# Optimization experiments

Hardware: AMD Instinct MI355X
Metric: run time of the kernel (lower is better)

Reference implementation:

```python
import jax, jax.numpy as jnp
import numpy as np

IN_F = 512
OUT_F = 512
ALPHA = 0.2  # LeakyReLU negative slope
# dropout p=0.1 is a no-op at inference (training=False), so omitted


def setup_inputs() -> dict:
    key = jax.random.key(0)
    k1, k2, k3 = jax.random.split(key, 3)
    B, N = 16, 1024
    x = jax.random.normal(k1, (B, N, IN_F), dtype=jnp.float32)
    # xavier_uniform with gain=1.414
    limW = 1.414 * np.sqrt(6.0 / (IN_F + OUT_F))
    W = jax.random.uniform(k2, (IN_F, OUT_F), minval=-limW, maxval=limW, dtype=jnp.float32)
    lima = 1.414 * np.sqrt(6.0 / (2 * OUT_F + 1))
    a = jax.random.uniform(k3, (2 * OUT_F, 1), minval=-lima, maxval=lima, dtype=jnp.float32)
    beta = jnp.ones((1,), dtype=jnp.float32)
    return {"x": x, "W": W, "a": a, "beta": beta}


def reference(x, W, a, beta):
    # h: [B, N, F]
    h = jnp.matmul(x, W)
    # Split attention vector: e_ij = leakyrelu(h_i . a1 + h_j . a2)
    a1 = a[:OUT_F, 0]   # [F]
    a2 = a[OUT_F:, 0]   # [F]
    s1 = jnp.einsum('bnf,f->bn', h, a1)  # [B, N]
    s2 = jnp.einsum('bnf,f->bn', h, a2)  # [B, N]
    e = s1[:, :, None] + s2[:, None, :]  # [B, N, N]
    e = jnp.where(e > 0, e, ALPHA * e)   # LeakyReLU
    attention = jax.nn.softmax(e, axis=2)
    h_prime = jnp.einsum('bnm,bmf->bnf', attention, h)
    out = jax.nn.elu(h_prime + beta * h)
    return out
```

## Files before the change

kernel.cpp:

```cpp
#include <hip/hip_runtime.h>

using u16 = unsigned short;
using u32 = unsigned int;

#define ALPHA 0.2f
#define LOG2E 1.4426950408889634f

typedef __bf16 bf16x8 __attribute__((ext_vector_type(8)));
typedef float f32x4 __attribute__((ext_vector_type(4)));
typedef float f32x16 __attribute__((ext_vector_type(16)));

__device__ __forceinline__ u16 f2bf(float f) {
  u32 u = __builtin_bit_cast(u32, f);
  u += 0x7FFFu + ((u >> 16) & 1u);
  return (u16)(u >> 16);
}
__device__ __forceinline__ float bf2f(u16 h) {
  u32 u = ((u32)h) << 16;
  return __builtin_bit_cast(float, u);
}
__device__ __forceinline__ void gload_lds16(const void* g, void* l) {
  __builtin_amdgcn_global_load_lds((__attribute__((address_space(1))) void*)g,
                                   (__attribute__((address_space(3))) void*)l,
                                   16, 0, 0);
}

__global__ __launch_bounds__(256) void k_cast_wT(const float* __restrict__ W, u16* __restrict__ wbt) {
  int idx = blockIdx.x * 256 + threadIdx.x;
  int k = idx >> 9, n = idx & 511;
  wbt[n * 512 + k] = f2bf(W[idx]);
}


__global__ __launch_bounds__(256, 2) void k_gemm1(const float* __restrict__ x, const u16* __restrict__ wbt,
                                                  const float* __restrict__ a,
                                                  u16* __restrict__ hbf, u16* __restrict__ hbt2,
                                                  float* __restrict__ s1p, float* __restrict__ s2p) {
  __shared__ __attribute__((aligned(16))) char lds[73728];
  __shared__ __attribute__((aligned(16))) float a_l[256];

  const int t = threadIdx.x;
  const int lane = t & 63;
  const int w = t >> 6;
  const int l31 = lane & 31, lhi = lane >> 5;
  const int rb = w >> 1, cg = w & 1;
  const int g = blockIdx.x;
  const int cb = (g >> 3) & 3;
  const int tile_m = (g & 7) | ((g >> 5) << 3);
  const int row0 = tile_m * 128;
  const int col0 = cb * 128;

  a_l[t] = (t < 128) ? a[col0 + t] : a[512 + col0 + (t - 128)];

  f32x16 acc[2][2];
#pragma unroll
  for (int i = 0; i < 2; ++i)
#pragma unroll
    for (int j = 0; j < 2; ++j)
#pragma unroll
      for (int r = 0; r < 16; ++r) acc[i][j][r] = 0.f;

#define STAGE_G1(kt, Ab, Bb)                                                              \
  {                                                                                       \
    const int k0_ = (kt) * 32;                                                            \
    _Pragma("unroll")                                                                     \
    for (int i = 0; i < 4; ++i) {                                                         \
      int G = i * 256 + t;                                                                \
      int row = G >> 3, ks = G & 7;                                                       \
      gload_lds16(x + (size_t)(row0 + row) * 512 + k0_ + ((ks ^ (row & 7)) * 4),          \
                  (Ab) + (size_t)(i * 256 + w * 64) * 16);                                \
    }                                                                                     \
    _Pragma("unroll")                                                                     \
    for (int i = 0; i < 2; ++i) {                                                         \
      int G = i * 256 + t;                                                                \
      int col = G >> 2, ks = G & 3;                                                       \
      gload_lds16(wbt + (size_t)(col0 + col) * 512 + k0_ + ((ks ^ ((col >> 1) & 3)) * 8), \
                  (Bb) + (size_t)(i * 256 + w * 64) * 16);                                \
    }                                                                                     \
  }

#define COMPUTE_G1(Ab, Bb)                                                                         \
  {                                                                                                \
    _Pragma("unroll")                                                                              \
    for (int ks = 0; ks < 2; ++ks) {                                                               \
      bf16x8 af[2];                                                                                \
      _Pragma("unroll")                                                                            \
      for (int sub = 0; sub < 2; ++sub) {                                                          \
        const int arow = rb * 64 + sub * 32 + l31;                                                 \
        const int kg = ks * 4 + lhi * 2;                                                           \
        f32x4 fa0 = *reinterpret_cast<const f32x4*>((Ab) + (size_t)(arow * 8 + (kg ^ (arow & 7))) * 16); \
        f32x4 fa1 = *reinterpret_cast<const f32x4*>((Ab) + (size_t)(arow * 8 + ((kg + 1) ^ (arow & 7))) * 16); \
        _Pragma("unroll")                                                                          \
        for (int jj = 0; jj < 4; ++jj) {                                                           \
          af[sub][jj] = (__bf16)fa0[jj];                                                           \
          af[sub][jj + 4] = (__bf16)fa1[jj];                                                       \
        }                                                                                          \
      }                                                                                            \
      bf16x8 bfr[2];                                                                               \
      _Pragma("unroll")                                                                            \
      for (int bt = 0; bt < 2; ++bt) {                                                             \
        const int bcol = cg * 64 + bt * 32 + l31;                                                  \
        const int kslot = (ks * 2 + lhi) ^ ((bcol >> 1) & 3);                                      \
        bfr[bt] = *reinterpret_cast<const bf16x8*>((Bb) + (size_t)(bcol * 4 + kslot) * 16);        \
      }                                                                                            \
      _Pragma("unroll")                                                                            \
      for (int sub = 0; sub < 2; ++sub)                                                            \
        _Pragma("unroll")                                                                          \
        for (int bt = 0; bt < 2; ++bt)                                                             \
          acc[sub][bt] = __builtin_amdgcn_mfma_f32_32x32x16_bf16(af[sub], bfr[bt], acc[sub][bt], 0, 0, 0); \
    }                                                                                              \
  }

  char* Ac = lds;             char* Bc = lds + 49152;
  char* An = lds + 16384;     char* Bn = lds + 57344;
  char* As = lds + 32768;     char* Bs = lds + 65536;

  STAGE_G1(0, Ac, Bc);
  STAGE_G1(1, An, Bn);
  __builtin_amdgcn_sched_barrier(0);
  asm volatile("s_waitcnt vmcnt(6) lgkmcnt(0)" ::: "memory");
  __builtin_amdgcn_s_barrier();
  __builtin_amdgcn_sched_barrier(0);

#pragma unroll 1
  for (int kt = 0; kt < 14; ++kt) {
    STAGE_G1(kt + 2, As, Bs);
    COMPUTE_G1(Ac, Bc);
    __builtin_amdgcn_sched_barrier(0);
    asm volatile("s_waitcnt vmcnt(6)" ::: "memory");
    __builtin_amdgcn_s_barrier();
    __builtin_amdgcn_sched_barrier(0);
    char* ta = Ac; Ac = An; An = As; As = ta;
    char* tb = Bc; Bc = Bn; Bn = Bs; Bs = tb;
  }
  COMPUTE_G1(Ac, Bc);
  __builtin_amdgcn_sched_barrier(0);
  asm volatile("s_waitcnt vmcnt(0)" ::: "memory");
  __builtin_amdgcn_s_barrier();
  __builtin_amdgcn_sched_barrier(0);
  COMPUTE_G1(An, Bn);
#undef STAGE_G1
#undef COMPUTE_G1

  __syncthreads();

  u16* lT = (u16*)lds;
#pragma unroll
  for (int sub = 0; sub < 2; ++sub)
#pragma unroll
    for (int bt = 0; bt < 2; ++bt) {
      const int col = cg * 64 + bt * 32 + l31;
#pragma unroll
      for (int r = 0; r < 16; ++r) {
        int row = rb * 64 + sub * 32 + (r & 3) + 8 * (r >> 2) + 4 * lhi;
        lT[row * 136 + col] = f2bf(acc[sub][bt][r]);
      }
    }
  __syncthreads();

#pragma unroll
  for (int i = 0; i < 8; ++i) {
    int G = i * 256 + t;
    int row = G >> 4, gg = G & 15;
    uint4 v = *reinterpret_cast<const uint4*>(&lT[row * 136 + gg * 8]);
    *reinterpret_cast<uint4*>(&hbf[(size_t)(row0 + row) * 512 + col0 + gg * 8]) = v;
  }
  const int bb = row0 >> 10;
  const int nb = row0 & 1023;
  u16* hb2 = hbt2 + (size_t)bb * 524288;
#pragma unroll
  for (int i = 0; i < 8; ++i) {
    int G = i * 256 + t;
    int col = G & 127, rg = G >> 7;
    u32 wd[4];
#pragma unroll
    for (int jj = 0; jj < 4; ++jj) {
      u16 lo = lT[(rg * 8 + 2 * jj) * 136 + col];
      u16 hi = lT[(rg * 8 + 2 * jj + 1) * 136 + col];
      wd[jj] = (u32)lo | ((u32)hi << 16);
    }
    uint4 o = {wd[0], wd[1], wd[2], wd[3]};
    const int m0 = nb + rg * 8;
    const int f = col0 + col;
    size_t idx = (size_t)(m0 >> 4) * 8192 + (size_t)(f >> 5) * 512 + (size_t)((m0 >> 3) & 1) * 256 + (size_t)(f & 31) * 8;
    *reinterpret_cast<uint4*>(&hb2[idx]) = o;
  }
  {
    const int r2 = t >> 1, half = t & 1;
    float d1 = 0.f, d2 = 0.f;
#pragma unroll
    for (int i = 0; i < 8; ++i) {
      uint4 v = *reinterpret_cast<const uint4*>(&lT[r2 * 136 + half * 64 + i * 8]);
      u32 wds[4] = {v.x, v.y, v.z, v.w};
#pragma unroll
      for (int jj = 0; jj < 8; ++jj) {
        float h = bf2f((u16)(wds[jj >> 1] >> ((jj & 1) * 16)));
        d1 += h * a_l[half * 64 + i * 8 + jj];
        d2 += h * a_l[128 + half * 64 + i * 8 + jj];
      }
    }
    d1 += __shfl_xor(d1, 1);
    d2 += __shfl_xor(d2, 1);
    if (half == 0) {
      s1p[cb * 16384 + row0 + r2] = d1;
      s2p[cb * 16384 + row0 + r2] = d2;
    }
  }
}

__global__ __launch_bounds__(256) void k_reduce(const float* __restrict__ s1p, const float* __restrict__ s2p,
                                                float* __restrict__ s1L, float* __restrict__ s2L) {
  int id = blockIdx.x * 256 + threadIdx.x;
  float d1 = s1p[id] + s1p[16384 + id] + s1p[32768 + id] + s1p[49152 + id];
  float d2 = s2p[id] + s2p[16384 + id] + s2p[32768 + id] + s2p[49152 + id];
  s1L[id] = d1 * LOG2E;
  s2L[id] = d2 * LOG2E;
}

__global__ __launch_bounds__(256, 2) void k_attn(const u16* __restrict__ hbt2, const u16* __restrict__ hbf,
                                                 const float* __restrict__ s1Lg, const float* __restrict__ s2Lg,
                                                 const float* __restrict__ betag, float* __restrict__ out) {
  __shared__ __attribute__((aligned(16))) float e1_l[1024];
  __shared__ __attribute__((aligned(16))) float e2_l[1024];
  const int t = threadIdx.x;
  const int lane = t & 63;
  const int w = t >> 6;
  const int l31 = lane & 31, lhi = lane >> 5;

  const int B = blockIdx.x;
  const int b = (B & 7) * 2 + ((B >> 3) & 1);
  const int j = B >> 4;
  const int n0 = (j >> 2) * 128;
  const int c0 = (j & 3) * 128;

  const u16* hb2 = hbt2 + (size_t)b * 524288;

  for (int i = t; i < 1024; i += 256) {
    float v = s2Lg[b * 1024 + i];
    e1_l[i] = exp2f(v);
    e2_l[i] = exp2f(ALPHA * v);
  }

  const int myrow = n0 + w * 32 + l31;
  const float s1v = s1Lg[b * 1024 + myrow];
  const float c1 = exp2f(s1v), c2 = exp2f(ALPHA * s1v);

  f32x16 acc[4];
#pragma unroll
  for (int ct = 0; ct < 4; ++ct)
#pragma unroll
    for (int r = 0; r < 16; ++r) acc[ct][r] = 0.f;
  f32x16 accs;
#pragma unroll
  for (int r = 0; r < 16; ++r) accs[r] = 0.f;
  bf16x8 ones;
#pragma unroll
  for (int q = 0; q < 8; ++q) ones[q] = (__bf16)1.0f;

  __syncthreads();

  const u16* bp = hb2 + (size_t)(c0 >> 5) * 512 + (size_t)(lhi * 32 + l31) * 8;

#define LOAD_B(dst, s)                                                                         \
  {                                                                                            \
    const u16* np_ = bp + (size_t)(s) * 8192;                                                  \
    _Pragma("unroll")                                                                          \
    for (int ct = 0; ct < 4; ++ct) dst[ct] = *reinterpret_cast<const bf16x8*>(np_ + ct * 512); \
  }

#define STEP_ATTN(s, buf)                                                      \
  {                                                                            \
    const int mo = (s) * 16 + lhi * 8;                                         \
    f32x4 ea = *reinterpret_cast<const f32x4*>(&e1_l[mo]);                     \
    f32x4 eb = *reinterpret_cast<const f32x4*>(&e1_l[mo + 4]);                 \
    f32x4 fa = *reinterpret_cast<const f32x4*>(&e2_l[mo]);                     \
    f32x4 fb = *reinterpret_cast<const f32x4*>(&e2_l[mo + 4]);                 \
    bf16x8 af;                                                                 \
    _Pragma("unroll")                                                          \
    for (int q = 0; q < 4; ++q) {                                              \
      af[q] = (__bf16)fmaxf(c1 * ea[q], c2 * fa[q]);                           \
      af[q + 4] = (__bf16)fmaxf(c1 * eb[q], c2 * fb[q]);                       \
    }                                                                          \
    accs = __builtin_amdgcn_mfma_f32_32x32x16_bf16(af, ones, accs, 0, 0, 0);   \
    _Pragma("unroll")                                                          \
    for (int ct = 0; ct < 4; ++ct)                                             \
      acc[ct] = __builtin_amdgcn_mfma_f32_32x32x16_bf16(af, (buf)[ct], acc[ct], 0, 0, 0); \
  }

  bf16x8 P0[4], P1[4], P2[4], P3[4], P4[4], P5[4], P6[4], P7[4];
  LOAD_B(P0, 0); LOAD_B(P1, 1); LOAD_B(P2, 2); LOAD_B(P3, 3);
  LOAD_B(P4, 4); LOAD_B(P5, 5); LOAD_B(P6, 6); LOAD_B(P7, 7);

#pragma unroll 1
  for (int s = 0; s < 56; s += 8) {
    STEP_ATTN(s + 0, P0); LOAD_B(P0, s + 8);
    STEP_ATTN(s + 1, P1); LOAD_B(P1, s + 9);
    STEP_ATTN(s + 2, P2); LOAD_B(P2, s + 10);
    STEP_ATTN(s + 3, P3); LOAD_B(P3, s + 11);
    STEP_ATTN(s + 4, P4); LOAD_B(P4, s + 12);
    STEP_ATTN(s + 5, P5); LOAD_B(P5, s + 13);
    STEP_ATTN(s + 6, P6); LOAD_B(P6, s + 14);
    STEP_ATTN(s + 7, P7); LOAD_B(P7, s + 15);
  }
  STEP_ATTN(56, P0); STEP_ATTN(57, P1); STEP_ATTN(58, P2); STEP_ATTN(59, P3);
  STEP_ATTN(60, P4); STEP_ATTN(61, P5); STEP_ATTN(62, P6); STEP_ATTN(63, P7);
#undef LOAD_B
#undef STEP_ATTN

  const float beta = betag[0];
  const u16* hf = hbf + (size_t)b * 1024 * 512;
#pragma unroll
  for (int rg = 0; rg < 4; ++rg) {
    f32x4 iv;
#pragma unroll
    for (int q = 0; q < 4; ++q) iv[q] = 1.0f / accs[rg * 4 + q];
#pragma unroll
    for (int ct = 0; ct < 4; ++ct) {
      const int colv = c0 + ct * 32 + l31;
      const int rowb = n0 + w * 32 + rg * 8 + lhi * 4;
#pragma unroll
      for (int q = 0; q < 4; ++q) {
        float hv = bf2f(hf[(size_t)(rowb + q) * 512 + colv]);
        float xv = acc[ct][rg * 4 + q] * iv[q] + beta * hv;
        out[((size_t)b * 1024 + rowb + q) * 512 + colv] = xv > 0.f ? xv : __expf(xv) - 1.0f;
      }
    }
  }
}

extern "C" void kernel_launch(void* const* d_in, const int* in_sizes, int n_in,
                              void* d_out, int out_size, void* d_ws, size_t ws_size,
                              hipStream_t stream) {
  const float* x = (const float*)d_in[0];
  const float* W = (const float*)d_in[1];
  const float* a = (const float*)d_in[2];
  const float* beta = (const float*)d_in[3];
  float* out = (float*)d_out;

  char* ws = (char*)d_ws;
  u16* hbf = (u16*)ws;
  u16* hbt2 = (u16*)(ws + (16u << 20));
  u16* wbt = (u16*)(ws + (32u << 20));
  float* s1p = (float*)(ws + (32u << 20) + (512u << 10));
  float* s2p = (float*)(ws + (32u << 20) + (768u << 10));
  float* s1L = (float*)(ws + (33u << 20));
  float* s2L = (float*)(ws + (33u << 20) + (64u << 10));

  k_cast_wT<<<1024, 256, 0, stream>>>(W, wbt);
  k_gemm1<<<512, 256, 0, stream>>>(x, wbt, a, hbf, hbt2, s1p, s2p);
  k_reduce<<<64, 256, 0, stream>>>(s1p, s2p, s1L, s2L);
  k_attn<<<512, 256, 0, stream>>>(hbt2, hbf, s1L, s2L, beta, out);
}
```

Before: 67.16 us.

## Switch attention kernel to 16x16x32 MFMA with smaller row tiles and more blocks

The attention-aggregation kernel moves from 32x32x16 to 16x16x32 bf16 MFMA. Each block now covers 64 rows instead of 128, so the grid doubles to 1024 blocks. The prefetch ring shrinks from 8 to 3 stages and the occupancy hint rises from 2 to 3 blocks per CU, aiming for better latency hiding and load balance across CUs. The cost is that each block re-reads the full B operand for half as many rows, which doubles global/L2 traffic for h.

```diff
diff --git a/kernel.cpp b/kernel.cpp
--- a/kernel.cpp
+++ b/kernel.cpp
@@ -217,7 +217,7 @@
   s2L[id] = d2 * LOG2E;
 }
 
-__global__ __launch_bounds__(256, 2) void k_attn(const u16* __restrict__ hbt2, const u16* __restrict__ hbf,
+__global__ __launch_bounds__(256, 3) void k_attn(const u16* __restrict__ hbt2, const u16* __restrict__ hbf,
                                                  const float* __restrict__ s1Lg, const float* __restrict__ s2Lg,
                                                  const float* __restrict__ betag, float* __restrict__ out) {
   __shared__ __attribute__((aligned(16))) float e1_l[1024];
@@ -225,12 +225,13 @@
   const int t = threadIdx.x;
   const int lane = t & 63;
   const int w = t >> 6;
-  const int l31 = lane & 31, lhi = lane >> 5;
+  const int fl = lane & 15;
+  const int mg = lane >> 4;
 
   const int B = blockIdx.x;
   const int b = (B & 7) * 2 + ((B >> 3) & 1);
   const int j = B >> 4;
-  const int n0 = (j >> 2) * 128;
+  const int n0 = (j >> 2) * 64;
   const int c0 = (j & 3) * 128;
 
   const u16* hb2 = hbt2 + (size_t)b * 524288;
@@ -241,89 +242,80 @@
     e2_l[i] = exp2f(ALPHA * v);
   }
 
-  const int myrow = n0 + w * 32 + l31;
+  const int myrow = n0 + w * 16 + fl;
   const float s1v = s1Lg[b * 1024 + myrow];
   const float c1 = exp2f(s1v), c2 = exp2f(ALPHA * s1v);
 
-  f32x16 acc[4];
-#pragma unroll
-  for (int ct = 0; ct < 4; ++ct)
-#pragma unroll
-    for (int r = 0; r < 16; ++r) acc[ct][r] = 0.f;
-  f32x16 accs;
-#pragma unroll
-  for (int r = 0; r < 16; ++r) accs[r] = 0.f;
+  f32x4 acc[8];
+#pragma unroll
+  for (int ct = 0; ct < 8; ++ct) acc[ct] = (f32x4){0.f, 0.f, 0.f, 0.f};
+  f32x4 accs = (f32x4){0.f, 0.f, 0.f, 0.f};
   bf16x8 ones;
 #pragma unroll
   for (int q = 0; q < 8; ++q) ones[q] = (__bf16)1.0f;
 
   __syncthreads();
 
-  const u16* bp = hb2 + (size_t)(c0 >> 5) * 512 + (size_t)(lhi * 32 + l31) * 8;
-
-#define LOAD_B(dst, s)                                                                         \
-  {                                                                                            \
-    const u16* np_ = bp + (size_t)(s) * 8192;                                                  \
-    _Pragma("unroll")                                                                          \
-    for (int ct = 0; ct < 4; ++ct) dst[ct] = *reinterpret_cast<const bf16x8*>(np_ + ct * 512); \
-  }
-
-#define STEP_ATTN(s, buf)                                                      \
-  {                                                                            \
-    const int mo = (s) * 16 + lhi * 8;                                         \
-    f32x4 ea = *reinterpret_cast<const f32x4*>(&e1_l[mo]);                     \
-    f32x4 eb = *reinterpret_cast<const f32x4*>(&e1_l[mo + 4]);                 \
-    f32x4 fa = *reinterpret_cast<const f32x4*>(&e2_l[mo]);                     \
-    f32x4 fb = *reinterpret_cast<const f32x4*>(&e2_l[mo + 4]);                 \
-    bf16x8 af;                                                                 \
-    _Pragma("unroll")                                                          \
-    for (int q = 0; q < 4; ++q) {                                              \
-      af[q] = (__bf16)fmaxf(c1 * ea[q], c2 * fa[q]);                           \
-      af[q + 4] = (__bf16)fmaxf(c1 * eb[q], c2 * fb[q]);                       \
-    }                                                                          \
-    accs = __builtin_amdgcn_mfma_f32_32x32x16_bf16(af, ones, accs, 0, 0, 0);   \
-    _Pragma("unroll")                                                          \
-    for (int ct = 0; ct < 4; ++ct)                                             \
-      acc[ct] = __builtin_amdgcn_mfma_f32_32x32x16_bf16(af, (buf)[ct], acc[ct], 0, 0, 0); \
-  }
-
-  bf16x8 P0[4], P1[4], P2[4], P3[4], P4[4], P5[4], P6[4], P7[4];
-  LOAD_B(P0, 0); LOAD_B(P1, 1); LOAD_B(P2, 2); LOAD_B(P3, 3);
-  LOAD_B(P4, 4); LOAD_B(P5, 5); LOAD_B(P6, 6); LOAD_B(P7, 7);
+  const u16* bp = hb2 + (size_t)(c0 >> 5) * 512 + (size_t)(mg >> 1) * 8192 + (size_t)(mg & 1) * 256 + (size_t)fl * 8;
+  const int mgo = mg * 8;
+
+#define LOAD_B(dst, s)                                                                          \
+  {                                                                                             \
+    const u16* np_ = bp + (size_t)(s) * 16384;                                                  \
+    _Pragma("unroll")                                                                           \
+    for (int ct = 0; ct < 8; ++ct)                                                              \
+      dst[ct] = *reinterpret_cast<const bf16x8*>(np_ + (ct >> 1) * 512 + (ct & 1) * 128);       \
+  }
+
+#define STEP_ATTN(s, buf)                                                       \
+  {                                                                             \
+    const int mo = (s) * 32 + mgo;                                              \
+    f32x4 ea = *reinterpret_cast<const f32x4*>(&e1_l[mo]);                      \
+    f32x4 eb = *reinterpret_cast<const f32x4*>(&e1_l[mo + 4]);                  \
+    f32x4 fa = *reinterpret_cast<const f32x4*>(&e2_l[mo]);                      \
+    f32x4 fb = *reinterpret_cast<const f32x4*>(&e2_l[mo + 4]);                  \
+    bf16x8 af;                                                                  \
+    _Pragma("unroll")                                                           \
+    for (int q = 0; q < 4; ++q) {                                               \
+      af[q] = (__bf16)fmaxf(c1 * ea[q], c2 * fa[q]);                            \
+      af[q + 4] = (__bf16)fmaxf(c1 * eb[q], c2 * fb[q]);                        \
+    }                                                                           \
+    accs = __builtin_amdgcn_mfma_f32_16x16x32_bf16(af, ones, accs, 0, 0, 0);    \
+    _Pragma("unroll")                                                           \
+    for (int ct = 0; ct < 8; ++ct)                                              \
+      acc[ct] = __builtin_amdgcn_mfma_f32_16x16x32_bf16(af, (buf)[ct], acc[ct], 0, 0, 0); \
+  }
+
+  bf16x8 P0[8], P1[8], P2[8];
+  LOAD_B(P0, 0);
+  LOAD_B(P1, 1);
+  LOAD_B(P2, 2);
 
 #pragma unroll 1
-  for (int s = 0; s < 56; s += 8) {
-    STEP_ATTN(s + 0, P0); LOAD_B(P0, s + 8);
-    STEP_ATTN(s + 1, P1); LOAD_B(P1, s + 9);
-    STEP_ATTN(s + 2, P2); LOAD_B(P2, s + 10);
-    STEP_ATTN(s + 3, P3); LOAD_B(P3, s + 11);
-    STEP_ATTN(s + 4, P4); LOAD_B(P4, s + 12);
-    STEP_ATTN(s + 5, P5); LOAD_B(P5, s + 13);
-    STEP_ATTN(s + 6, P6); LOAD_B(P6, s + 14);
-    STEP_ATTN(s + 7, P7); LOAD_B(P7, s + 15);
-  }
-  STEP_ATTN(56, P0); STEP_ATTN(57, P1); STEP_ATTN(58, P2); STEP_ATTN(59, P3);
-  STEP_ATTN(60, P4); STEP_ATTN(61, P5); STEP_ATTN(62, P6); STEP_ATTN(63, P7);
+  for (int s = 0; s < 30; s += 3) {
+    STEP_ATTN(s + 0, P0); LOAD_B(P0, (s + 3) & 31);
+    STEP_ATTN(s + 1, P1); LOAD_B(P1, (s + 4) & 31);
+    STEP_ATTN(s + 2, P2); LOAD_B(P2, (s + 5) & 31);
+  }
+  STEP_ATTN(30, P0);
+  STEP_ATTN(31, P1);
 #undef LOAD_B
 #undef STEP_ATTN
 
   const float beta = betag[0];
   const u16* hf = hbf + (size_t)b * 1024 * 512;
-#pragma unroll
-  for (int rg = 0; rg < 4; ++rg) {
-    f32x4 iv;
-#pragma unroll
-    for (int q = 0; q < 4; ++q) iv[q] = 1.0f / accs[rg * 4 + q];
-#pragma unroll
-    for (int ct = 0; ct < 4; ++ct) {
-      const int colv = c0 + ct * 32 + l31;
-      const int rowb = n0 + w * 32 + rg * 8 + lhi * 4;
-#pragma unroll
-      for (int q = 0; q < 4; ++q) {
-        float hv = bf2f(hf[(size_t)(rowb + q) * 512 + colv]);
-        float xv = acc[ct][rg * 4 + q] * iv[q] + beta * hv;
-        out[((size_t)b * 1024 + rowb + q) * 512 + colv] = xv > 0.f ? xv : __expf(xv) - 1.0f;
-      }
+  f32x4 iv;
+#pragma unroll
+  for (int q = 0; q < 4; ++q) iv[q] = 1.0f / accs[q];
+  const int rowb = n0 + w * 16 + (lane >> 4) * 4;
+#pragma unroll
+  for (int ct = 0; ct < 8; ++ct) {
+    const int colv = c0 + ct * 16 + fl;
+#pragma unroll
+    for (int q = 0; q < 4; ++q) {
+      float hv = bf2f(hf[(size_t)(rowb + q) * 512 + colv]);
+      float xv = acc[ct][q] * iv[q] + beta * hv;
+      out[((size_t)b * 1024 + rowb + q) * 512 + colv] = xv > 0.f ? xv : __expf(xv) - 1.0f;
     }
   }
 }
@@ -349,5 +341,5 @@
   k_cast_wT<<<1024, 256, 0, stream>>>(W, wbt);
   k_gemm1<<<512, 256, 0, stream>>>(x, wbt, a, hbf, hbt2, s1p, s2p);
   k_reduce<<<64, 256, 0, stream>>>(s1p, s2p, s1L, s2L);
-  k_attn<<<512, 256, 0, stream>>>(hbt2, hbf, s1L, s2L, beta, out);
-}
+  k_attn<<<1024, 256, 0, stream>>>(hbt2, hbf, s1L, s2L, beta, out);
+}
```

Result: no change. 67.81 us (+1.0%).
